# Kernel tuning notes

Hardware: AMD Instinct MI355X
Metric: run time of the kernel (lower is better)

## Reference

```python
import jax, jax.numpy as jnp
import numpy as np

B, S, D_IN, D_OUT, N, R = 8, 4096, 1280, 1280, 4, 16


def setup_inputs() -> dict:
    key = jax.random.key(0)
    ks = jax.random.split(key, 7)
    x = jax.random.normal(ks[0], (B, S, D_IN), dtype=jnp.float32)
    W = jax.random.normal(ks[1], (D_OUT, D_IN), dtype=jnp.float32) * 0.02
    bias = jax.random.normal(ks[2], (D_OUT,), dtype=jnp.float32) * 0.02
    A = jax.random.normal(ks[3], (N, R, D_IN), dtype=jnp.float32) * 0.02
    Bw = jax.random.normal(ks[4], (N, D_OUT, R), dtype=jnp.float32) * 0.02
    scalings = jax.random.uniform(ks[5], (N,), dtype=jnp.float32)
    masks = jax.random.uniform(ks[6], (N, S), dtype=jnp.float32)
    # normalize masks to sum ~1 per position, per docstring
    masks = masks / jnp.sum(masks, axis=0, keepdims=True)
    return {"x": x, "W": W, "bias": bias, "A": A, "Bw": Bw,
            "scalings": scalings, "masks": masks}


def reference(x, W, bias, A, Bw, scalings, masks):
    # base linear: y = x @ W^T + b
    base = jnp.einsum('bsd,od->bso', x, W) + bias
    # batched LoRA branches: h = x @ A_i^T  (b,s,n,r)
    h = jnp.einsum('bsd,nrd->bsnr', x, A)
    # lora_out_i = h @ B_i^T  (b,s,n,o)
    lora = jnp.einsum('bsnr,nor->bsno', h, Bw)
    # weighted sum over subjects: scaling_i * mask_i(pos)
    lora_sum = jnp.einsum('bsno,n,ns->bso', lora, scalings, masks)
    return base + lora_sum
```

## Files before the change

kernel.cpp:

```cpp
#include <hip/hip_runtime.h>
#include <hip/hip_bf16.h>
#include <stdint.h>

#define S_LEN   4096
#define DIN     1280
#define DOUT    1280
#define N_LORA  4
#define R_LORA  16
#define M_TOT   32768
#define KC      (DIN + N_LORA*R_LORA)
#define NR      64

typedef __attribute__((ext_vector_type(4))) float floatx4;
typedef __attribute__((ext_vector_type(8))) short shortx8;

static __device__ __forceinline__ unsigned short bf16_rne(float f) {
    union { float f; unsigned u; } v; v.f = f;
    unsigned u = v.u;
    u += 0x7fffu + ((u >> 16) & 1u);
    return (unsigned short)(u >> 16);
}

static __device__ __forceinline__ void async16(const unsigned short* g, unsigned short* l) {
    __builtin_amdgcn_global_load_lds(
        (const __attribute__((address_space(1))) unsigned int*)g,
        (__attribute__((address_space(3))) unsigned int*)l, 16, 0, 0);
}

static __device__ __forceinline__ uint4 cvt8(const float* src) {
    const float4* p = (const float4*)src;
    float4 a = p[0], b = p[1];
    uint4 o;
    o.x = (unsigned)bf16_rne(a.x) | ((unsigned)bf16_rne(a.y) << 16);
    o.y = (unsigned)bf16_rne(a.z) | ((unsigned)bf16_rne(a.w) << 16);
    o.z = (unsigned)bf16_rne(b.x) | ((unsigned)bf16_rne(b.y) << 16);
    o.w = (unsigned)bf16_rne(b.z) | ((unsigned)bf16_rne(b.w) << 16);
    return o;
}

#define VMCNT(n) asm volatile("s_waitcnt vmcnt(" #n ")" ::: "memory")
#define LGKM0    do { asm volatile("s_waitcnt lgkmcnt(0)" ::: "memory"); \
                      __builtin_amdgcn_sched_barrier(0); } while (0)
static __device__ __forceinline__ void barx() {
    asm volatile("" ::: "memory");
    __builtin_amdgcn_s_barrier();
    asm volatile("" ::: "memory");
}

__global__ __launch_bounds__(256) void k_convert_x(const float* __restrict__ x,
                                                   unsigned short* __restrict__ xb) {
    size_t e = ((size_t)blockIdx.x * 256 + threadIdx.x) * 8;
    *(uint4*)(xb + e) = cvt8(x + e);
}

__global__ __launch_bounds__(256) void k_build_wcat(const float* __restrict__ W,
                                                    const float* __restrict__ Bw,
                                                    unsigned short* __restrict__ Wcat) {
    int i = blockIdx.x * 256 + threadIdx.x;
    int e = i * 8;
    int o = e / KC;
    int c = e - o * KC;
    const float* src;
    if (c < DIN) {
        src = W + o * DIN + c;
    } else {
        int j = c - DIN;
        int n = j >> 4, r = j & 15;
        src = Bw + (n * DOUT + o) * R_LORA + r;
    }
    *(uint4*)(Wcat + o * KC + c) = cvt8(src);
}

__global__ __launch_bounds__(256) void k_convert_abp(const float* __restrict__ A,
                                                     unsigned short* __restrict__ Abp) {
    int step = blockIdx.x;
    int t = threadIdx.x;
    int ct = t >> 6, lane = t & 63;
    int mi = lane & 15, kq = lane >> 4;
    const float* src = A + (ct * 16 + mi) * DIN + step * 32 + kq * 8;
    *(uint4*)(Abp + ((size_t)(step * 4 + ct) * 64 + lane) * 8) = cvt8(src);
}

__global__ __launch_bounds__(1024) void k_lora_g(const unsigned short* __restrict__ xb,
                                                 const unsigned short* __restrict__ Abp,
                                                 const float* __restrict__ scalings,
                                                 const float* __restrict__ masks,
                                                 unsigned short* __restrict__ g) {
    __shared__ float hs[4][64][64];
    int tid = threadIdx.x;
    int wave = tid >> 6, lane = tid & 63;
    int kg = wave >> 2, wv = wave & 3;
    int mi = lane & 15, kq = lane >> 4;
    int m0 = blockIdx.x * 64;

    const unsigned short* xrow = xb + (size_t)(m0 + wv * 16 + mi) * DIN;

    floatx4 acc[4] = {};
    for (int s = 0; s < 10; ++s) {
        int step = kg * 10 + s;
        int k = step * 32 + kq * 8;
        shortx8 xf = *(const shortx8*)(xrow + k);
#pragma unroll
        for (int ct = 0; ct < 4; ++ct) {
            shortx8 bfr = *(const shortx8*)(Abp + ((size_t)(step * 4 + ct) * 64 + lane) * 8);
            acc[ct] = __builtin_amdgcn_mfma_f32_16x16x32_bf16(xf, bfr, acc[ct], 0, 0, 0);
        }
    }
#pragma unroll
    for (int ct = 0; ct < 4; ++ct)
#pragma unroll
        for (int reg = 0; reg < 4; ++reg)
            hs[kg][wv * 16 + kq * 4 + reg][ct * 16 + mi] = acc[ct][reg];
    __syncthreads();

    int r = tid >> 4;
    int c0 = (tid & 15) * 4;
    float4 s0 = *(const float4*)&hs[0][r][c0];
    float4 s1 = *(const float4*)&hs[1][r][c0];
    float4 s2 = *(const float4*)&hs[2][r][c0];
    float4 s3 = *(const float4*)&hs[3][r][c0];
    int n = c0 >> 4;
    int m = m0 + r;
    float wgt = scalings[n] * masks[n * S_LEN + (m & (S_LEN - 1))];
    float v0 = (s0.x + s1.x + s2.x + s3.x) * wgt;
    float v1 = (s0.y + s1.y + s2.y + s3.y) * wgt;
    float v2 = (s0.z + s1.z + s2.z + s3.z) * wgt;
    float v3 = (s0.w + s1.w + s2.w + s3.w) * wgt;
    uint2 packed;
    packed.x = (unsigned)bf16_rne(v0) | ((unsigned)bf16_rne(v1) << 16);
    packed.y = (unsigned)bf16_rne(v2) | ((unsigned)bf16_rne(v3) << 16);
    *(uint2*)(g + (size_t)m * NR + c0) = packed;
}

__global__ __launch_bounds__(512, 2) void k_main_gemm(const unsigned short* __restrict__ xb,
                                                      const unsigned short* __restrict__ g,
                                                      const unsigned short* __restrict__ Wcat,
                                                      const float* __restrict__ bias,
                                                      float* __restrict__ out) {
    __shared__ alignas(16) unsigned short As[2][256 * 64];
    __shared__ alignas(16) unsigned short Bs[2][256 * 64];

    const int tid = threadIdx.x;
    const int wave = tid >> 6, lane = tid & 63;
    const int wm = wave >> 2, wn = wave & 3;
    const int mi = lane & 15, kq = lane >> 4;

    int bx = blockIdx.x;
    int xcd = bx & 7, slot = bx >> 3;
    int srb = slot / 5;
    const int m0 = (xcd * 16 + srb) * 256;
    const int n0 = (slot - srb * 5) * 256;

    const int tr = tid >> 3;
    const int ts = (tid & 7) ^ (tr & 7);

    const unsigned short* pA = xb   + (size_t)(m0 + tr) * DIN + ts * 8;
    const unsigned short* pG = g    + (size_t)(m0 + tr) * NR  + ts * 8;
    const unsigned short* pB = Wcat + (size_t)(n0 + tr) * KC  + ts * 8;

    const int swz  = mi & 7;
    const int loK0 = mi * 128 + (((0) + kq) ^ swz) * 16;
    const int loK1 = mi * 128 + (((4) + kq) ^ swz) * 16;
    const int rbA  = (wm * 128) * 128;
    const int rbB  = (wn * 64) * 128;

    floatx4 acc[8][4] = {};
    shortx8 aR[2][8];
    shortx8 b[2][4];

    auto stA = [&](int t, int h) {
        unsigned short* d = &As[t & 1][(h * 128) * 64 + tid * 8];
        if (t < 20) {
            const unsigned short* s = pA + (size_t)(h * 128) * DIN + t * 64;
            async16(s, d);
            async16(s + (size_t)64 * DIN, d + 64 * 64);
        } else {
            const unsigned short* s = pG + (size_t)(h * 128) * NR;
            async16(s, d);
            async16(s + (size_t)64 * NR, d + 64 * 64);
        }
    };
    auto stB = [&](int t, int h) {
        const unsigned short* s = pB + (size_t)(h * 128) * KC + t * 64;
        unsigned short* d = &Bs[t & 1][(h * 128) * 64 + tid * 8];
        async16(s, d);
        async16(s + (size_t)64 * KC, d + 64 * 64);
    };

#define READ_A(bufb, mh)  _Pragma("unroll") \
    for (int fm = 0; fm < 4; ++fm) { \
        const char* p = (const char*)As[bufb] + rbA + ((mh) * 64 + fm * 16) * 128; \
        aR[(mh)][fm * 2 + 0] = *(const shortx8*)(p + loK0); \
        aR[(mh)][fm * 2 + 1] = *(const shortx8*)(p + loK1); \
    }
#define READ_B(bufb, nh)  _Pragma("unroll") \
    for (int fn = 0; fn < 2; ++fn) { \
        const char* p = (const char*)Bs[bufb] + rbB + ((nh) * 32 + fn * 16) * 128; \
        b[nh][fn * 2 + 0] = *(const shortx8*)(p + loK0); \
        b[nh][fn * 2 + 1] = *(const shortx8*)(p + loK1); \
    }
#define MFMA16(mh, nh)  do { __builtin_amdgcn_s_setprio(1); \
    _Pragma("unroll") \
    for (int fm = 0; fm < 4; ++fm) \
        _Pragma("unroll") \
        for (int fn = 0; fn < 2; ++fn) { \
            acc[(mh)*4+fm][(nh)*2+fn] = __builtin_amdgcn_mfma_f32_16x16x32_bf16( \
                aR[(mh)][fm*2+0], b[nh][fn*2+0], acc[(mh)*4+fm][(nh)*2+fn], 0, 0, 0); \
            acc[(mh)*4+fm][(nh)*2+fn] = __builtin_amdgcn_mfma_f32_16x16x32_bf16( \
                aR[(mh)][fm*2+1], b[nh][fn*2+1], acc[(mh)*4+fm][(nh)*2+fn], 0, 0, 0); \
        } \
    __builtin_amdgcn_s_setprio(0); } while (0)

    stA(0, 0); stA(0, 1); stB(0, 0); stB(0, 1);
    stB(1, 0); stB(1, 1); stA(1, 0); stA(1, 1);
    VMCNT(8);
    barx();
    READ_A(0, 0); READ_B(0, 0);

    for (int it = 0; it < 10; ++it) {
        const int N0 = 2 * it + 2, N1 = 2 * it + 3;
        const bool lastI = (it == 9);

        barx(); LGKM0;
        READ_B(0, 1);
        MFMA16(0, 0);
        barx();
        barx(); LGKM0;
        READ_A(0, 1);
        MFMA16(0, 1);
        barx();
        stB(N0, 0);
        barx(); LGKM0;
        MFMA16(1, 0);
        barx();
        stB(N0, 1); stA(N0, 0);
        barx(); VMCNT(6); LGKM0;
        READ_A(1, 0); READ_B(1, 0);
        MFMA16(1, 1);
        barx();
        stA(N0, 1);
        barx(); LGKM0;
        READ_B(1, 1);
        MFMA16(0, 0);
        barx();
        barx(); LGKM0;
        READ_A(1, 1);
        MFMA16(0, 1);
        barx();
        if (!lastI) stB(N1, 0);
        barx(); LGKM0;
        MFMA16(1, 0);
        barx();
        if (!lastI) { stB(N1, 1); stA(N1, 0); }
        barx();
        if (lastI) { VMCNT(0); } else { VMCNT(6); }
        LGKM0;
        READ_A(0, 0); READ_B(0, 0);
        MFMA16(1, 1);
        barx();
        if (!lastI) stA(N1, 1);
    }

    LGKM0;
    READ_B(0, 1);
    MFMA16(0, 0);
    LGKM0;
    READ_A(0, 1);
    MFMA16(0, 1);
    LGKM0;
    MFMA16(1, 0);
    MFMA16(1, 1);

    float bv[4];
#pragma unroll
    for (int nf = 0; nf < 4; ++nf)
        bv[nf] = bias[n0 + wn * 64 + (nf >> 1) * 32 + (nf & 1) * 16 + mi];
#pragma unroll
    for (int mf = 0; mf < 8; ++mf) {
        const int row = m0 + wm * 128 + (mf >> 2) * 64 + (mf & 3) * 16 + kq * 4;
#pragma unroll
        for (int nf = 0; nf < 4; ++nf) {
            const int col = n0 + wn * 64 + (nf >> 1) * 32 + (nf & 1) * 16 + mi;
            float* op = out + (size_t)row * DOUT + col;
#pragma unroll
            for (int reg = 0; reg < 4; ++reg)
                op[(size_t)reg * DOUT] = acc[mf][nf][reg] + bv[nf];
        }
    }
#undef READ_A
#undef READ_B
#undef MFMA16
}

extern "C" void kernel_launch(void* const* d_in, const int* in_sizes, int n_in,
                              void* d_out, int out_size, void* d_ws, size_t ws_size,
                              hipStream_t stream) {
    const float* x     = (const float*)d_in[0];
    const float* W     = (const float*)d_in[1];
    const float* bias  = (const float*)d_in[2];
    const float* A     = (const float*)d_in[3];
    const float* Bw    = (const float*)d_in[4];
    const float* scal  = (const float*)d_in[5];
    const float* masks = (const float*)d_in[6];
    float* out = (float*)d_out;

    unsigned short* xb   = (unsigned short*)d_ws;
    unsigned short* g    = xb + (size_t)M_TOT * DIN;
    unsigned short* Wcat = g + (size_t)M_TOT * NR;
    unsigned short* Abp  = Wcat + (size_t)DOUT * KC;

    k_convert_x<<<(M_TOT * DIN) / (8 * 256), 256, 0, stream>>>(x, xb);
    k_build_wcat<<<(DOUT * KC) / (8 * 256), 256, 0, stream>>>(W, Bw, Wcat);
    k_convert_abp<<<DIN / 32, 256, 0, stream>>>(A, Abp);
    k_lora_g<<<M_TOT / 64, 1024, 0, stream>>>(xb, Abp, scal, masks, g);
    k_main_gemm<<<(M_TOT / 256) * (DOUT / 256), 512, 0, stream>>>(xb, g, Wcat, bias, out);
}
```

Baseline: 436.6 us.

## Fuse x bf16 conversion into LoRA kernel and tighten main GEMM barrier schedule

Removes the standalone fp32-to-bf16 conversion kernel for x. The LoRA projection kernel now reads fp32 x, converts it in registers, writes the bf16 copy for the main GEMM and feeds it straight to the MFMA. This saves one full read of x and a kernel launch. The main GEMM loop is also rescheduled: redundant back-to-back barriers are removed, one A-tile store is moved earlier, and the vmcnt waits are retuned. That reduces barrier stalls but risks LDS hazards if the new wait counts are too loose.

```diff
diff --git a/kernel.cpp b/kernel.cpp
--- a/kernel.cpp
+++ b/kernel.cpp
@@ -13,6 +13,8 @@
 
 typedef __attribute__((ext_vector_type(4))) float floatx4;
 typedef __attribute__((ext_vector_type(8))) short shortx8;
+
+typedef union { uint4 u; shortx8 s; } punx8;
 
 static __device__ __forceinline__ unsigned short bf16_rne(float f) {
     union { float f; unsigned u; } v; v.f = f;
@@ -45,12 +47,6 @@
     asm volatile("" ::: "memory");
     __builtin_amdgcn_s_barrier();
     asm volatile("" ::: "memory");
-}
-
-__global__ __launch_bounds__(256) void k_convert_x(const float* __restrict__ x,
-                                                   unsigned short* __restrict__ xb) {
-    size_t e = ((size_t)blockIdx.x * 256 + threadIdx.x) * 8;
-    *(uint4*)(xb + e) = cvt8(x + e);
 }
 
 __global__ __launch_bounds__(256) void k_build_wcat(const float* __restrict__ W,
@@ -81,11 +77,12 @@
     *(uint4*)(Abp + ((size_t)(step * 4 + ct) * 64 + lane) * 8) = cvt8(src);
 }
 
-__global__ __launch_bounds__(1024) void k_lora_g(const unsigned short* __restrict__ xb,
+__global__ __launch_bounds__(1024) void k_lora_g(const float* __restrict__ x,
                                                  const unsigned short* __restrict__ Abp,
                                                  const float* __restrict__ scalings,
                                                  const float* __restrict__ masks,
-                                                 unsigned short* __restrict__ g) {
+                                                 unsigned short* __restrict__ g,
+                                                 unsigned short* __restrict__ xb) {
     __shared__ float hs[4][64][64];
     int tid = threadIdx.x;
     int wave = tid >> 6, lane = tid & 63;
@@ -93,13 +90,16 @@
     int mi = lane & 15, kq = lane >> 4;
     int m0 = blockIdx.x * 64;
 
-    const unsigned short* xrow = xb + (size_t)(m0 + wv * 16 + mi) * DIN;
+    const float* xrow = x + (size_t)(m0 + wv * 16 + mi) * DIN;
+    unsigned short* xbrow = xb + (size_t)(m0 + wv * 16 + mi) * DIN;
 
     floatx4 acc[4] = {};
     for (int s = 0; s < 10; ++s) {
         int step = kg * 10 + s;
         int k = step * 32 + kq * 8;
-        shortx8 xf = *(const shortx8*)(xrow + k);
+        punx8 xp; xp.u = cvt8(xrow + k);
+        *(uint4*)(xbrow + k) = xp.u;
+        shortx8 xf = xp.s;
 #pragma unroll
         for (int ct = 0; ct < 4; ++ct) {
             shortx8 bfr = *(const shortx8*)(Abp + ((size_t)(step * 4 + ct) * 64 + lane) * 8);
@@ -212,53 +212,53 @@
     __builtin_amdgcn_s_setprio(0); } while (0)
 
     stA(0, 0); stA(0, 1); stB(0, 0); stB(0, 1);
-    stB(1, 0); stB(1, 1); stA(1, 0); stA(1, 1);
-    VMCNT(8);
+    stB(1, 0); stB(1, 1); stA(1, 0);
+    VMCNT(6);
     barx();
     READ_A(0, 0); READ_B(0, 0);
 
     for (int it = 0; it < 10; ++it) {
-        const int N0 = 2 * it + 2, N1 = 2 * it + 3;
+        const int T1 = 2 * it + 1, N0 = 2 * it + 2, N1 = 2 * it + 3;
         const bool lastI = (it == 9);
 
-        barx(); LGKM0;
+        barx();
+        stA(T1, 1);
+        LGKM0;
         READ_B(0, 1);
         MFMA16(0, 0);
         barx();
-        barx(); LGKM0;
+        LGKM0;
         READ_A(0, 1);
         MFMA16(0, 1);
         barx();
         stB(N0, 0);
-        barx(); LGKM0;
+        LGKM0;
         MFMA16(1, 0);
+        VMCNT(2);
         barx();
         stB(N0, 1); stA(N0, 0);
-        barx(); VMCNT(6); LGKM0;
+        LGKM0;
         READ_A(1, 0); READ_B(1, 0);
         MFMA16(1, 1);
         barx();
         stA(N0, 1);
-        barx(); LGKM0;
+        LGKM0;
         READ_B(1, 1);
         MFMA16(0, 0);
         barx();
-        barx(); LGKM0;
+        LGKM0;
         READ_A(1, 1);
         MFMA16(0, 1);
         barx();
         if (!lastI) stB(N1, 0);
-        barx(); LGKM0;
+        LGKM0;
         MFMA16(1, 0);
+        if (lastI) { VMCNT(0); } else { VMCNT(2); }
         barx();
         if (!lastI) { stB(N1, 1); stA(N1, 0); }
-        barx();
-        if (lastI) { VMCNT(0); } else { VMCNT(6); }
         LGKM0;
         READ_A(0, 0); READ_B(0, 0);
         MFMA16(1, 1);
-        barx();
-        if (!lastI) stA(N1, 1);
     }
 
     LGKM0;
@@ -309,9 +309,8 @@
     unsigned short* Wcat = g + (size_t)M_TOT * NR;
     unsigned short* Abp  = Wcat + (size_t)DOUT * KC;
 
-    k_convert_x<<<(M_TOT * DIN) / (8 * 256), 256, 0, stream>>>(x, xb);
     k_build_wcat<<<(DOUT * KC) / (8 * 256), 256, 0, stream>>>(W, Bw, Wcat);
     k_convert_abp<<<DIN / 32, 256, 0, stream>>>(A, Abp);
-    k_lora_g<<<M_TOT / 64, 1024, 0, stream>>>(xb, Abp, scal, masks, g);
+    k_lora_g<<<M_TOT / 64, 1024, 0, stream>>>(x, Abp, scal, masks, g, xb);
     k_main_gemm<<<(M_TOT / 256) * (DOUT / 256), 512, 0, stream>>>(xb, g, Wcat, bias, out);
 }
```

Result: slower. 455.2 us (+4.3%).
